# Kernel optimization log

Hardware: AMD Instinct MI355X
Metric: run time of the kernel (lower is better)

## Reference

```python
import jax, jax.numpy as jnp
import numpy as np

N_NODES = 50000
N_EDGES = 800000
FEAT_DIM = 64
NUM_RELS = 8


def setup_inputs() -> dict:
    key = jax.random.key(0)
    k1, k2, k3, k4, k5 = jax.random.split(key, 5)
    features = jax.random.normal(k1, (N_NODES, FEAT_DIM), dtype=jnp.float32)
    # xavier_uniform with relu gain ~= sqrt(2)*sqrt(6/(D+D))
    limit = np.sqrt(2.0) * np.sqrt(6.0 / (FEAT_DIM + FEAT_DIM))
    weight_r = jax.random.uniform(k2, (NUM_RELS, FEAT_DIM, FEAT_DIM), dtype=jnp.float32,
                                  minval=-limit, maxval=limit)
    src = jax.random.randint(k3, (N_EDGES,), 0, N_NODES, dtype=jnp.int64 if jax.config.jax_enable_x64 else jnp.int32)
    dst = jax.random.randint(k4, (N_EDGES,), 0, N_NODES, dtype=src.dtype)
    etype = jax.random.randint(k5, (N_EDGES,), 0, NUM_RELS, dtype=src.dtype)
    return {"features": features, "weight_r": weight_r, "src": src, "dst": dst, "etype": etype}


def reference(features, weight_r, src, dst, etype):
    N, D = features.shape
    c = 0.2
    # in-degree of each destination node (DGL 'deg' node data)
    deg = jax.ops.segment_sum(jnp.ones(dst.shape, dtype=features.dtype), dst, num_segments=N)
    # relation-batched matmul: h @ W_r for every relation, then gather per edge.
    # [R, N, D] = 8*50000*64 floats -- cheap vs. materializing [E, D, D] weights.
    hw = jnp.einsum('nd,rdf->rnf', features, weight_r)
    msg = hw[etype, src] / deg[dst][:, None]          # [E, D]
    M = jax.ops.segment_sum(msg, dst, num_segments=N)  # scatter-sum mailbox reduce
    updated = jax.nn.relu(c * features + (1.0 - c) * M)
    # DGL only applies reduce to nodes that received messages; others keep h.
    return jnp.where((deg > 0)[:, None], updated, features)
```

## Files before the change

### kernel.cpp

```cpp
#include <hip/hip_runtime.h>
#include <hip/hip_bf16.h>

#define N_NODES 50000
#define N_EDGES 800000
#define FEAT 64
#define NRELS 8
#define NBUCK 391
#define NBP 196
#define BCAP 2816
#define FB_BLOCKS 782
#define NPB 32
#define FUSE_BLOCKS 1563

typedef __attribute__((ext_vector_type(8))) short bf16x8;
typedef __attribute__((ext_vector_type(4))) float f32x4;

static __host__ __device__ inline size_t align256(size_t x) { return (x + 255) & ~(size_t)255; }

__device__ inline unsigned short f2b(float f) {
    unsigned u = __builtin_bit_cast(unsigned, f);
    unsigned r = (u + 0x7fffu + ((u >> 16) & 1u)) >> 16;
    return (unsigned short)r;
}
__device__ inline float b2f(unsigned short u) {
    unsigned v = ((unsigned)u) << 16;
    return __builtin_bit_cast(float, v);
}

__global__ void bfill_kernel(const int* __restrict__ dst, const int* __restrict__ srcv,
                             const int* __restrict__ et, const float* __restrict__ W,
                             const float* __restrict__ feat,
                             int* __restrict__ bcnt, int* __restrict__ tmp,
                             unsigned short* __restrict__ WtT,
                             unsigned short* __restrict__ Fb, int E, int N) {
    const int t = threadIdx.x;

    if (blockIdx.x >= NBP) {
        const int fbb = blockIdx.x - NBP;
        if (fbb < 32) {
            int i4 = fbb * 256 + t;
            float4 v = ((const float4*)W)[i4];
            int bse = i4 * 4;
            int f0 = bse & 63;
            int rd = bse >> 6;
            int d  = rd & 63;
            int r  = rd >> 6;
            unsigned short* w0 = WtT + ((size_t)(r * 64 + f0) * 64 + d);
            w0[0 * 64] = f2b(v.x);
            w0[1 * 64] = f2b(v.y);
            w0[2 * 64] = f2b(v.z);
            w0[3 * 64] = f2b(v.w);
        }
        const int node = fbb * 64 + (t >> 2);
        if (node >= N) return;
        const int seg = t & 3;
        const float4* F4 = (const float4*)feat + (size_t)node * 16 + seg * 4;
        float4 v0 = F4[0], v1 = F4[1], v2 = F4[2], v3 = F4[3];
        bf16x8 b0, b1;
        b0[0] = (short)f2b(v0.x); b0[1] = (short)f2b(v0.y);
        b0[2] = (short)f2b(v0.z); b0[3] = (short)f2b(v0.w);
        b0[4] = (short)f2b(v1.x); b0[5] = (short)f2b(v1.y);
        b0[6] = (short)f2b(v1.z); b0[7] = (short)f2b(v1.w);
        b1[0] = (short)f2b(v2.x); b1[1] = (short)f2b(v2.y);
        b1[2] = (short)f2b(v2.z); b1[3] = (short)f2b(v2.w);
        b1[4] = (short)f2b(v3.x); b1[5] = (short)f2b(v3.y);
        b1[6] = (short)f2b(v3.z); b1[7] = (short)f2b(v3.w);
        *(bf16x8*)(Fb + (size_t)node * 64 + seg * 16)     = b0;
        *(bf16x8*)(Fb + (size_t)node * 64 + seg * 16 + 8) = b1;
        return;
    }

    __shared__ int hist[392];
    __shared__ int base[392];
    __shared__ int lcur[392];
    for (int j = t; j < 392; j += 256) { hist[j] = 0; lcur[j] = 0; }
    __syncthreads();

    const int4* dst4 = (const int4*)dst;
    const int4* src4 = (const int4*)srcv;
    const int4* et4  = (const int4*)et;
    const int n4 = E >> 2;
    int bk[16], pk[16];
#pragma unroll
    for (int k = 0; k < 4; k++) {
        int i4 = blockIdx.x * 1024 + t + k * 256;
        if (i4 < n4) {
            int4 d = dst4[i4];
            int4 s = src4[i4];
            int4 r = et4[i4];
            const int dd[4] = {d.x, d.y, d.z, d.w};
            const int ss[4] = {s.x, s.y, s.z, s.w};
            const int rr[4] = {r.x, r.y, r.z, r.w};
#pragma unroll
            for (int j = 0; j < 4; j++) {
                int idx = k * 4 + j;
                bk[idx] = dd[j] >> 7;
                pk[idx] = (ss[j] & 0xFFFF) | (rr[j] << 16) | ((dd[j] & 127) << 19);
                atomicAdd(&hist[bk[idx]], 1);
            }
        } else {
#pragma unroll
            for (int j = 0; j < 4; j++) bk[k * 4 + j] = -1;
        }
    }
    __syncthreads();
    for (int j = t; j < NBUCK; j += 256)
        if (hist[j] > 0)
            base[j] = j * BCAP + atomicAdd(&bcnt[j], hist[j]);
    __syncthreads();
#pragma unroll
    for (int k = 0; k < 16; k++) {
        if (bk[k] >= 0) {
            int r = atomicAdd(&lcur[bk[k]], 1);
            int pos = base[bk[k]] + r;
            if (pos < (bk[k] + 1) * BCAP)
                tmp[pos] = pk[k];
        }
    }
}

__global__ void mid_kernel(const int* __restrict__ bcnt, const int* __restrict__ tmp,
                           int* __restrict__ spk, int* __restrict__ off_s,
                           int* __restrict__ off_e, int N) {
    __shared__ int hist[1024];
    __shared__ int s[256];
    const int t = threadIdx.x;

    const int b = blockIdx.x;
    const int n0 = b * 128;
    const int nn = min(128, N - n0);
    const int s0 = b * BCAP;
    const int s1 = s0 + min(bcnt[b], BCAP);

    *(int4*)&hist[t * 4] = make_int4(0, 0, 0, 0);
    __syncthreads();
    for (int i = s0 + t; i < s1; i += 1024) {
        int v0 = tmp[i];
        int v1 = (i + 256 < s1) ? tmp[i + 256] : -1;
        int v2 = (i + 512 < s1) ? tmp[i + 512] : -1;
        int v3 = (i + 768 < s1) ? tmp[i + 768] : -1;
        atomicAdd(&hist[(v0 >> 16) & 1023], 1);
        if (v1 >= 0) atomicAdd(&hist[(v1 >> 16) & 1023], 1);
        if (v2 >= 0) atomicAdd(&hist[(v2 >> 16) & 1023], 1);
        if (v3 >= 0) atomicAdd(&hist[(v3 >> 16) & 1023], 1);
    }
    __syncthreads();
    int loc[4], st4[4], T = 0;
#pragma unroll
    for (int j = 0; j < 4; j++) loc[j] = hist[t * 4 + j];
#pragma unroll
    for (int j = 0; j < 4; j++) { st4[j] = T; T += loc[j]; }
    s[t] = T;
    __syncthreads();
    for (int o = 1; o < 256; o <<= 1) {
        int u = (t >= o) ? s[t - o] : 0;
        __syncthreads();
        s[t] += u;
        __syncthreads();
    }
    const int ex = s[t] - T;
    {
        const int n = t >> 1;
        if (n < nn) {
            if ((t & 1) == 0) off_s[n0 + n] = s0 + ex;
            else              off_e[n0 + n] = s0 + ex + T;
        }
    }
#pragma unroll
    for (int j = 0; j < 4; j++) hist[t * 4 + j] = s0 + ex + st4[j];
    __syncthreads();
    for (int i = s0 + t; i < s1; i += 1024) {
        int v0 = tmp[i];
        int v1 = (i + 256 < s1) ? tmp[i + 256] : -1;
        int v2 = (i + 512 < s1) ? tmp[i + 512] : -1;
        int v3 = (i + 768 < s1) ? tmp[i + 768] : -1;
        int p0 = atomicAdd(&hist[(v0 >> 16) & 1023], 1);
        spk[p0] = v0;
        if (v1 >= 0) { int p1 = atomicAdd(&hist[(v1 >> 16) & 1023], 1); spk[p1] = v1; }
        if (v2 >= 0) { int p2 = atomicAdd(&hist[(v2 >> 16) & 1023], 1); spk[p2] = v2; }
        if (v3 >= 0) { int p3 = atomicAdd(&hist[(v3 >> 16) & 1023], 1); spk[p3] = v3; }
    }
}

__global__ __launch_bounds__(256, 4) void fuse_kernel(
    const int* __restrict__ off_s, const int* __restrict__ off_e,
    const int* __restrict__ spk, const unsigned short* __restrict__ Fb,
    const unsigned short* __restrict__ WtT, const float* __restrict__ feat,
    float* __restrict__ out, int N) {
    __shared__ unsigned short Sb[NRELS][NPB][64];
    const int t = threadIdx.x;
    const int n0 = blockIdx.x * NPB;
    const int nn = min(NPB, N - n0);
    const int gid = t >> 3, q = t & 7;
    const int lanebase = (t & 63) & ~7;

    int b = 0, e = 0;
    if (gid < nn) {
        const int gn = n0 + gid;
        b = off_s[gn];
        e = off_e[gn];
    }

    float4 h0e = make_float4(0.f, 0.f, 0.f, 0.f), h1e = h0e;
    const int ef0 = q * 8;
    if (gid < nn) {
        const float4* fp = (const float4*)feat + (size_t)(n0 + gid) * 16 + (ef0 >> 2);
        h0e = fp[0];
        h1e = fp[1];
    }

    {
        f32x4 z = {0.f, 0.f, 0.f, 0.f};
        f32x4* zp = (f32x4*)&Sb[0][0][0];
#pragma unroll
        for (int i = 0; i < 8; i++) zp[t + 256 * i] = z;
    }
    __syncthreads();

    if (gid < nn && b < e) {
        const int swz = (q ^ (gid & 7)) * 8;
        unsigned short* srow = &Sb[0][0][0] + (size_t)gid * 64 + swz;
        float a[8] = {0.f, 0.f, 0.f, 0.f, 0.f, 0.f, 0.f, 0.f};
        int curR = -1;

        auto flushS = [&](int rel) {
            bf16x8 v;
#pragma unroll
            for (int k = 0; k < 8; k++) v[k] = (short)f2b(a[k]);
            *(bf16x8*)(srow + (size_t)rel * (NPB * 64)) = v;
        };

        int pks[4];
#pragma unroll
        for (int k = 0; k < 4; k++)
            pks[k] = (b + q + 8 * k < e) ? spk[b + q + 8 * k] : -1;

        bf16x8 u[8];
        int pkv[8];
#pragma unroll
        for (int j = 0; j < 8; j++) {
            int pk = __shfl(pks[0], lanebase | j);
            pkv[j] = pk;
            u[j] = (bf16x8){0, 0, 0, 0, 0, 0, 0, 0};
            if (pk >= 0)
                u[j] = *(const bf16x8*)(Fb + (size_t)(pk & 0xFFFF) * 64 + q * 8);
        }
#pragma unroll
        for (int tier = 0; tier < 4; tier++) {
            if (b + tier * 8 >= e) break;
#pragma unroll
            for (int jj = 0; jj < 8; jj++) {
                const int j = tier * 8 + jj;
                bf16x8 uu = u[jj];
                int pk = pkv[jj];
                if (tier < 3) {
                    int pkn = __shfl(pks[(j + 8) >> 3], lanebase | jj);
                    pkv[jj] = pkn;
                    if (pkn >= 0)
                        u[jj] = *(const bf16x8*)(Fb + (size_t)(pkn & 0xFFFF) * 64 + q * 8);
                }
                if (pk >= 0) {
                    int rel = (pk >> 16) & 7;
                    if (rel != curR) {
                        if (curR >= 0) flushS(curR);
                        curR = rel;
#pragma unroll
                        for (int k = 0; k < 8; k++) a[k] = b2f((unsigned short)uu[k]);
                    } else {
#pragma unroll
                        for (int k = 0; k < 8; k++) a[k] += b2f((unsigned short)uu[k]);
                    }
                }
            }
        }
        for (int i = b + 32; i < e; i++) {
            int pk = spk[i];
            bf16x8 uu = *(const bf16x8*)(Fb + (size_t)(pk & 0xFFFF) * 64 + q * 8);
            int rel = (pk >> 16) & 7;
            if (rel != curR) {
                if (curR >= 0) flushS(curR);
                curR = rel;
#pragma unroll
                for (int k = 0; k < 8; k++) a[k] = b2f((unsigned short)uu[k]);
            } else {
#pragma unroll
                for (int k = 0; k < 8; k++) a[k] += b2f((unsigned short)uu[k]);
            }
        }
        if (curR >= 0) flushS(curR);
    }
    __syncthreads();

    const int w = t >> 6, l = t & 63, col = l & 15, quad = l >> 4;
    f32x4 acc0 = {0.f, 0.f, 0.f, 0.f}, acc1 = {0.f, 0.f, 0.f, 0.f};
    const int sw0 = (quad ^ (col & 7)) * 8;
    const int sw1 = ((quad + 4) ^ (col & 7)) * 8;
#pragma unroll
    for (int r = 0; r < NRELS; r++) {
        const unsigned short* wp = WtT + (size_t)r * 4096 + ((w * 16 + col) * 64 + quad * 8);
        bf16x8 b0 = *(const bf16x8*)wp;
        bf16x8 b1 = *(const bf16x8*)(wp + 32);
        const unsigned short* Sr = &Sb[0][0][0] + (size_t)r * (NPB * 64);
        bf16x8 a0 = *(const bf16x8*)&Sr[col * 64 + sw0];
        bf16x8 a1 = *(const bf16x8*)&Sr[col * 64 + sw1];
        bf16x8 c0 = *(const bf16x8*)&Sr[(16 + col) * 64 + sw0];
        bf16x8 c1 = *(const bf16x8*)&Sr[(16 + col) * 64 + sw1];
        acc0 = __builtin_amdgcn_mfma_f32_16x16x32_bf16(a0, b0, acc0, 0, 0, 0);
        acc0 = __builtin_amdgcn_mfma_f32_16x16x32_bf16(a1, b1, acc0, 0, 0, 0);
        acc1 = __builtin_amdgcn_mfma_f32_16x16x32_bf16(c0, b0, acc1, 0, 0, 0);
        acc1 = __builtin_amdgcn_mfma_f32_16x16x32_bf16(c1, b1, acc1, 0, 0, 0);
    }
    __syncthreads();

    float* C = (float*)&Sb[0][0][0];
#pragma unroll
    for (int i = 0; i < 4; i++) {
        C[(quad * 4 + i) * 72 + w * 16 + col]        = acc0[i];
        C[(16 + quad * 4 + i) * 72 + w * 16 + col]   = acc1[i];
    }
    __syncthreads();

    if (gid < nn) {
        const int gn = n0 + gid;
        const int deg = e - b;
        float4 m0 = *(const float4*)&C[gid * 72 + ef0];
        float4 m1 = *(const float4*)&C[gid * 72 + ef0 + 4];
        float4 r0, r1;
        if (deg > 0) {
            float inv = 0.8f / (float)deg;
            r0.x = fmaxf(0.2f * h0e.x + m0.x * inv, 0.f);
            r0.y = fmaxf(0.2f * h0e.y + m0.y * inv, 0.f);
            r0.z = fmaxf(0.2f * h0e.z + m0.z * inv, 0.f);
            r0.w = fmaxf(0.2f * h0e.w + m0.w * inv, 0.f);
            r1.x = fmaxf(0.2f * h1e.x + m1.x * inv, 0.f);
            r1.y = fmaxf(0.2f * h1e.y + m1.y * inv, 0.f);
            r1.z = fmaxf(0.2f * h1e.z + m1.z * inv, 0.f);
            r1.w = fmaxf(0.2f * h1e.w + m1.w * inv, 0.f);
        } else {
            r0 = h0e; r1 = h1e;
        }
        float4* op = (float4*)out + (size_t)gn * 16 + (ef0 >> 2);
        op[0] = r0;
        op[1] = r1;
    }
}

__global__ void degf_kernel(const int* __restrict__ dst, float* __restrict__ deg, int E) {
    int e = blockIdx.x * blockDim.x + threadIdx.x;
    if (e < E) atomicAdd(deg + dst[e], 1.0f);
}

__global__ void otf_kernel(const int* __restrict__ src, const int* __restrict__ dst,
                           const int* __restrict__ et, const float* __restrict__ feat,
                           const float* __restrict__ W, float* __restrict__ out, int E) {
    int wid = (blockIdx.x * blockDim.x + threadIdx.x) >> 6;
    int l = threadIdx.x & 63;
    if (wid >= E) return;
    int s = src[wid], dd = dst[wid], r = et[wid];
    float fv = feat[(size_t)s * 64 + l];
    const float* Wr = W + (size_t)r * 4096;
    float acc = 0.f;
#pragma unroll
    for (int d = 0; d < 64; d++) {
        float a = __shfl(fv, d);
        acc += a * Wr[d * 64 + l];
    }
    atomicAdd(out + (size_t)dd * 64 + l, acc);
}

__global__ void final_kernel(const float* __restrict__ feat, const float* __restrict__ deg,
                             float* __restrict__ out, int N) {
    int i = blockIdx.x * blockDim.x + threadIdx.x;
    if (i >= N * 16) return;
    int n = i >> 4;
    float d = deg[n];
    float4 f = ((const float4*)feat)[i];
    float4 m = ((float4*)out)[i];
    float4 res;
    if (d > 0.f) {
        float inv = 0.8f / d;
        res.x = fmaxf(0.2f * f.x + m.x * inv, 0.f);
        res.y = fmaxf(0.2f * f.y + m.y * inv, 0.f);
        res.z = fmaxf(0.2f * f.z + m.z * inv, 0.f);
        res.w = fmaxf(0.2f * f.w + m.w * inv, 0.f);
    } else {
        res = f;
    }
    ((float4*)out)[i] = res;
}

extern "C" void kernel_launch(void* const* d_in, const int* in_sizes, int n_in,
                              void* d_out, int out_size, void* d_ws, size_t ws_size,
                              hipStream_t stream) {
    const float* feat = (const float*)d_in[0];
    const float* W    = (const float*)d_in[1];
    const int*   src  = (const int*)d_in[2];
    const int*   dst  = (const int*)d_in[3];
    const int*   et   = (const int*)d_in[4];
    float* out = (float*)d_out;

    const int N = N_NODES, E = N_EDGES;

    char* p = (char*)d_ws;
    int* bcnt  = (int*)p;  p += align256((size_t)NBUCK * 4);
    int* off_s = (int*)p;  p += align256((size_t)N * 4);
    int* off_e = (int*)p;  p += align256((size_t)N * 4);
    int* tmp   = (int*)p;  p += align256((size_t)NBUCK * BCAP * 4);
    int* spk   = (int*)p;  p += align256((size_t)NBUCK * BCAP * 4);
    unsigned short* WtT = (unsigned short*)p;
    p += align256((size_t)NRELS * FEAT * FEAT * 2);
    unsigned short* Fb = (unsigned short*)p;
    p += align256((size_t)N * FEAT * 2);
    size_t need_full = (size_t)(p - (char*)d_ws);

    if (ws_size >= need_full) {
        hipMemsetAsync(bcnt, 0, (size_t)NBUCK * 4, stream);
        bfill_kernel<<<NBP + FB_BLOCKS, 256, 0, stream>>>(dst, src, et, W, feat,
                                                          bcnt, tmp, WtT, Fb, E, N);
        mid_kernel<<<NBUCK, 256, 0, stream>>>(bcnt, tmp, spk, off_s, off_e, N);
        fuse_kernel<<<FUSE_BLOCKS, 256, 0, stream>>>(off_s, off_e, spk, Fb, WtT,
                                                     feat, out, N);
    } else {
        float* deg = (float*)d_ws;
        hipMemsetAsync(out, 0, (size_t)N * FEAT * 4, stream);
        hipMemsetAsync(deg, 0, (size_t)N * 4, stream);
        degf_kernel<<<(E + 255) / 256, 256, 0, stream>>>(dst, deg, E);
        otf_kernel<<<(E + 3) / 4, 256, 0, stream>>>(src, dst, et, feat, W, out, E);
        final_kernel<<<(N * 16 + 255) / 256, 256, 0, stream>>>(feat, deg, out, N);
    }
}
```

Before: 129.9 us.

## Fuse per-bucket counting sort into aggregation kernel with 32-node buckets

Buckets shrink to 32 destination nodes each, which matches the fused block size. The separate mid_kernel counting sort is removed: each fuse block now reads its bucket from tmp, histograms by (node, relation) in shared memory, scatters the edges into an LDS edge list, and aggregates directly. This drops one kernel launch and the global round trip through spk/off arrays. The cost is a larger per-block LDS footprint and more shared-memory atomics on 1563 buckets in bfill. BCAP=768 per bucket could overflow for a skewed dst distribution, and edges past the cap would be silently dropped.

```diff
diff --git a/kernel.cpp b/kernel.cpp
--- a/kernel.cpp
+++ b/kernel.cpp
@@ -5,12 +5,11 @@
 #define N_EDGES 800000
 #define FEAT 64
 #define NRELS 8
-#define NBUCK 391
+#define NPB 32
+#define NBUCK 1563
 #define NBP 196
-#define BCAP 2816
+#define BCAP 768
 #define FB_BLOCKS 782
-#define NPB 32
-#define FUSE_BLOCKS 1563
 
 typedef __attribute__((ext_vector_type(8))) short bf16x8;
 typedef __attribute__((ext_vector_type(4))) float f32x4;
@@ -70,10 +69,10 @@
         return;
     }
 
-    __shared__ int hist[392];
-    __shared__ int base[392];
-    __shared__ int lcur[392];
-    for (int j = t; j < 392; j += 256) { hist[j] = 0; lcur[j] = 0; }
+    __shared__ int hist[NBUCK];
+    __shared__ int base[NBUCK];
+    __shared__ int lcur[NBUCK];
+    for (int j = t; j < NBUCK; j += 256) { hist[j] = 0; lcur[j] = 0; }
     __syncthreads();
 
     const int4* dst4 = (const int4*)dst;
@@ -94,8 +93,8 @@
 #pragma unroll
             for (int j = 0; j < 4; j++) {
                 int idx = k * 4 + j;
-                bk[idx] = dd[j] >> 7;
-                pk[idx] = (ss[j] & 0xFFFF) | (rr[j] << 16) | ((dd[j] & 127) << 19);
+                bk[idx] = dd[j] >> 5;
+                pk[idx] = (ss[j] & 0xFFFF) | (rr[j] << 16) | ((dd[j] & 31) << 19);
                 atomicAdd(&hist[bk[idx]], 1);
             }
         } else {
@@ -119,86 +118,117 @@
     }
 }
 
-__global__ void mid_kernel(const int* __restrict__ bcnt, const int* __restrict__ tmp,
-                           int* __restrict__ spk, int* __restrict__ off_s,
-                           int* __restrict__ off_e, int N) {
-    __shared__ int hist[1024];
-    __shared__ int s[256];
-    const int t = threadIdx.x;
-
-    const int b = blockIdx.x;
-    const int n0 = b * 128;
-    const int nn = min(128, N - n0);
-    const int s0 = b * BCAP;
-    const int s1 = s0 + min(bcnt[b], BCAP);
-
-    *(int4*)&hist[t * 4] = make_int4(0, 0, 0, 0);
-    __syncthreads();
-    for (int i = s0 + t; i < s1; i += 1024) {
-        int v0 = tmp[i];
-        int v1 = (i + 256 < s1) ? tmp[i + 256] : -1;
-        int v2 = (i + 512 < s1) ? tmp[i + 512] : -1;
-        int v3 = (i + 768 < s1) ? tmp[i + 768] : -1;
-        atomicAdd(&hist[(v0 >> 16) & 1023], 1);
-        if (v1 >= 0) atomicAdd(&hist[(v1 >> 16) & 1023], 1);
-        if (v2 >= 0) atomicAdd(&hist[(v2 >> 16) & 1023], 1);
-        if (v3 >= 0) atomicAdd(&hist[(v3 >> 16) & 1023], 1);
-    }
-    __syncthreads();
-    int loc[4], st4[4], T = 0;
-#pragma unroll
-    for (int j = 0; j < 4; j++) loc[j] = hist[t * 4 + j];
-#pragma unroll
-    for (int j = 0; j < 4; j++) { st4[j] = T; T += loc[j]; }
-    s[t] = T;
-    __syncthreads();
-    for (int o = 1; o < 256; o <<= 1) {
-        int u = (t >= o) ? s[t - o] : 0;
-        __syncthreads();
-        s[t] += u;
-        __syncthreads();
-    }
-    const int ex = s[t] - T;
-    {
-        const int n = t >> 1;
-        if (n < nn) {
-            if ((t & 1) == 0) off_s[n0 + n] = s0 + ex;
-            else              off_e[n0 + n] = s0 + ex + T;
-        }
-    }
-#pragma unroll
-    for (int j = 0; j < 4; j++) hist[t * 4 + j] = s0 + ex + st4[j];
-    __syncthreads();
-    for (int i = s0 + t; i < s1; i += 1024) {
-        int v0 = tmp[i];
-        int v1 = (i + 256 < s1) ? tmp[i + 256] : -1;
-        int v2 = (i + 512 < s1) ? tmp[i + 512] : -1;
-        int v3 = (i + 768 < s1) ? tmp[i + 768] : -1;
-        int p0 = atomicAdd(&hist[(v0 >> 16) & 1023], 1);
-        spk[p0] = v0;
-        if (v1 >= 0) { int p1 = atomicAdd(&hist[(v1 >> 16) & 1023], 1); spk[p1] = v1; }
-        if (v2 >= 0) { int p2 = atomicAdd(&hist[(v2 >> 16) & 1023], 1); spk[p2] = v2; }
-        if (v3 >= 0) { int p3 = atomicAdd(&hist[(v3 >> 16) & 1023], 1); spk[p3] = v3; }
-    }
-}
-
 __global__ __launch_bounds__(256, 4) void fuse_kernel(
-    const int* __restrict__ off_s, const int* __restrict__ off_e,
-    const int* __restrict__ spk, const unsigned short* __restrict__ Fb,
+    const int* __restrict__ bcnt, const int* __restrict__ tmp,
+    const unsigned short* __restrict__ Fb,
     const unsigned short* __restrict__ WtT, const float* __restrict__ feat,
     float* __restrict__ out, int N) {
     __shared__ unsigned short Sb[NRELS][NPB][64];
+    __shared__ int sedge[BCAP];
+    __shared__ int hist[256];
+    __shared__ int noff[NPB + 1];
     const int t = threadIdx.x;
-    const int n0 = blockIdx.x * NPB;
+    const int bkt = blockIdx.x;
+    const int n0 = bkt * NPB;
     const int nn = min(NPB, N - n0);
     const int gid = t >> 3, q = t & 7;
-    const int lanebase = (t & 63) & ~7;
+
+    {
+        f32x4 z = {0.f, 0.f, 0.f, 0.f};
+        f32x4* zp = (f32x4*)&Sb[0][0][0];
+#pragma unroll
+        for (int i = 0; i < 8; i++) zp[t + 256 * i] = z;
+    }
+
+    const int cnt = min(bcnt[bkt], BCAP);
+    const int* tb = tmp + (size_t)bkt * BCAP;
+    hist[t] = 0;
+    __syncthreads();
+    int v0 = (t < cnt) ? tb[t] : -1;
+    int v1 = (t + 256 < cnt) ? tb[t + 256] : -1;
+    int v2 = (t + 512 < cnt) ? tb[t + 512] : -1;
+    if (v0 >= 0) atomicAdd(&hist[(v0 >> 16) & 255], 1);
+    if (v1 >= 0) atomicAdd(&hist[(v1 >> 16) & 255], 1);
+    if (v2 >= 0) atomicAdd(&hist[(v2 >> 16) & 255], 1);
+    __syncthreads();
+    const int myc = hist[t];
+    for (int o = 1; o < 256; o <<= 1) {
+        int u_ = (t >= o) ? hist[t - o] : 0;
+        __syncthreads();
+        hist[t] += u_;
+        __syncthreads();
+    }
+    const int ex = hist[t] - myc;
+    if ((t & 7) == 0) noff[t >> 3] = ex;
+    if (t == 255) noff[NPB] = ex + myc;
+    __syncthreads();
+    hist[t] = ex;
+    __syncthreads();
+    if (v0 >= 0) { int p = atomicAdd(&hist[(v0 >> 16) & 255], 1); sedge[p] = v0; }
+    if (v1 >= 0) { int p = atomicAdd(&hist[(v1 >> 16) & 255], 1); sedge[p] = v1; }
+    if (v2 >= 0) { int p = atomicAdd(&hist[(v2 >> 16) & 255], 1); sedge[p] = v2; }
+    __syncthreads();
 
     int b = 0, e = 0;
-    if (gid < nn) {
-        const int gn = n0 + gid;
-        b = off_s[gn];
-        e = off_e[gn];
+    if (gid < nn) { b = noff[gid]; e = noff[gid + 1]; }
+    if (gid < nn && b < e) {
+        const int swz = (q ^ (gid & 7)) * 8;
+        unsigned short* srow = &Sb[0][0][0] + (size_t)gid * 64 + swz;
+        float a[8] = {0.f, 0.f, 0.f, 0.f, 0.f, 0.f, 0.f, 0.f};
+        int curR = -1;
+
+        auto flushS = [&](int rel) {
+            bf16x8 v;
+#pragma unroll
+            for (int k = 0; k < 8; k++) v[k] = (short)f2b(a[k]);
+            *(bf16x8*)(srow + (size_t)rel * (NPB * 64)) = v;
+        };
+
+        int pkj[32];
+#pragma unroll
+        for (int j = 0; j < 32; j++) pkj[j] = (b + j < e) ? sedge[b + j] : -1;
+
+        bf16x8 u[8];
+#pragma unroll
+        for (int j = 0; j < 8; j++) {
+            u[j] = (bf16x8){0, 0, 0, 0, 0, 0, 0, 0};
+            if (pkj[j] >= 0)
+                u[j] = *(const bf16x8*)(Fb + (size_t)(pkj[j] & 0xFFFF) * 64 + q * 8);
+        }
+#pragma unroll
+        for (int j = 0; j < 32; j++) {
+            bf16x8 uu = u[j & 7];
+            if (j + 8 < 32 && pkj[j + 8] >= 0)
+                u[j & 7] = *(const bf16x8*)(Fb + (size_t)(pkj[j + 8] & 0xFFFF) * 64 + q * 8);
+            int pk = pkj[j];
+            if (pk >= 0) {
+                int rel = (pk >> 16) & 7;
+                if (rel != curR) {
+                    if (curR >= 0) flushS(curR);
+                    curR = rel;
+#pragma unroll
+                    for (int k = 0; k < 8; k++) a[k] = b2f((unsigned short)uu[k]);
+                } else {
+#pragma unroll
+                    for (int k = 0; k < 8; k++) a[k] += b2f((unsigned short)uu[k]);
+                }
+            }
+        }
+        for (int i = b + 32; i < e; i++) {
+            int pk = sedge[i];
+            bf16x8 uu = *(const bf16x8*)(Fb + (size_t)(pk & 0xFFFF) * 64 + q * 8);
+            int rel = (pk >> 16) & 7;
+            if (rel != curR) {
+                if (curR >= 0) flushS(curR);
+                curR = rel;
+#pragma unroll
+                for (int k = 0; k < 8; k++) a[k] = b2f((unsigned short)uu[k]);
+            } else {
+#pragma unroll
+                for (int k = 0; k < 8; k++) a[k] += b2f((unsigned short)uu[k]);
+            }
+        }
+        if (curR >= 0) flushS(curR);
     }
 
     float4 h0e = make_float4(0.f, 0.f, 0.f, 0.f), h1e = h0e;
@@ -207,87 +237,6 @@
         const float4* fp = (const float4*)feat + (size_t)(n0 + gid) * 16 + (ef0 >> 2);
         h0e = fp[0];
         h1e = fp[1];
-    }
-
-    {
-        f32x4 z = {0.f, 0.f, 0.f, 0.f};
-        f32x4* zp = (f32x4*)&Sb[0][0][0];
-#pragma unroll
-        for (int i = 0; i < 8; i++) zp[t + 256 * i] = z;
-    }
-    __syncthreads();
-
-    if (gid < nn && b < e) {
-        const int swz = (q ^ (gid & 7)) * 8;
-        unsigned short* srow = &Sb[0][0][0] + (size_t)gid * 64 + swz;
-        float a[8] = {0.f, 0.f, 0.f, 0.f, 0.f, 0.f, 0.f, 0.f};
-        int curR = -1;
-
-        auto flushS = [&](int rel) {
-            bf16x8 v;
-#pragma unroll
-            for (int k = 0; k < 8; k++) v[k] = (short)f2b(a[k]);
-            *(bf16x8*)(srow + (size_t)rel * (NPB * 64)) = v;
-        };
-
-        int pks[4];
-#pragma unroll
-        for (int k = 0; k < 4; k++)
-            pks[k] = (b + q + 8 * k < e) ? spk[b + q + 8 * k] : -1;
-
-        bf16x8 u[8];
-        int pkv[8];
-#pragma unroll
-        for (int j = 0; j < 8; j++) {
-            int pk = __shfl(pks[0], lanebase | j);
-            pkv[j] = pk;
-            u[j] = (bf16x8){0, 0, 0, 0, 0, 0, 0, 0};
-            if (pk >= 0)
-                u[j] = *(const bf16x8*)(Fb + (size_t)(pk & 0xFFFF) * 64 + q * 8);
-        }
-#pragma unroll
-        for (int tier = 0; tier < 4; tier++) {
-            if (b + tier * 8 >= e) break;
-#pragma unroll
-            for (int jj = 0; jj < 8; jj++) {
-                const int j = tier * 8 + jj;
-                bf16x8 uu = u[jj];
-                int pk = pkv[jj];
-                if (tier < 3) {
-                    int pkn = __shfl(pks[(j + 8) >> 3], lanebase | jj);
-                    pkv[jj] = pkn;
-                    if (pkn >= 0)
-                        u[jj] = *(const bf16x8*)(Fb + (size_t)(pkn & 0xFFFF) * 64 + q * 8);
-                }
-                if (pk >= 0) {
-                    int rel = (pk >> 16) & 7;
-                    if (rel != curR) {
-                        if (curR >= 0) flushS(curR);
-                        curR = rel;
-#pragma unroll
-                        for (int k = 0; k < 8; k++) a[k] = b2f((unsigned short)uu[k]);
-                    } else {
-#pragma unroll
-                        for (int k = 0; k < 8; k++) a[k] += b2f((unsigned short)uu[k]);
-                    }
-                }
-            }
-        }
-        for (int i = b + 32; i < e; i++) {
-            int pk = spk[i];
-            bf16x8 uu = *(const bf16x8*)(Fb + (size_t)(pk & 0xFFFF) * 64 + q * 8);
-            int rel = (pk >> 16) & 7;
-            if (rel != curR) {
-                if (curR >= 0) flushS(curR);
-                curR = rel;
-#pragma unroll
-                for (int k = 0; k < 8; k++) a[k] = b2f((unsigned short)uu[k]);
-            } else {
-#pragma unroll
-                for (int k = 0; k < 8; k++) a[k] += b2f((unsigned short)uu[k]);
-            }
-        }
-        if (curR >= 0) flushS(curR);
     }
     __syncthreads();
 
@@ -403,10 +352,7 @@
 
     char* p = (char*)d_ws;
     int* bcnt  = (int*)p;  p += align256((size_t)NBUCK * 4);
-    int* off_s = (int*)p;  p += align256((size_t)N * 4);
-    int* off_e = (int*)p;  p += align256((size_t)N * 4);
     int* tmp   = (int*)p;  p += align256((size_t)NBUCK * BCAP * 4);
-    int* spk   = (int*)p;  p += align256((size_t)NBUCK * BCAP * 4);
     unsigned short* WtT = (unsigned short*)p;
     p += align256((size_t)NRELS * FEAT * FEAT * 2);
     unsigned short* Fb = (unsigned short*)p;
@@ -417,9 +363,7 @@
         hipMemsetAsync(bcnt, 0, (size_t)NBUCK * 4, stream);
         bfill_kernel<<<NBP + FB_BLOCKS, 256, 0, stream>>>(dst, src, et, W, feat,
                                                           bcnt, tmp, WtT, Fb, E, N);
-        mid_kernel<<<NBUCK, 256, 0, stream>>>(bcnt, tmp, spk, off_s, off_e, N);
-        fuse_kernel<<<FUSE_BLOCKS, 256, 0, stream>>>(off_s, off_e, spk, Fb, WtT,
-                                                     feat, out, N);
+        fuse_kernel<<<NBUCK, 256, 0, stream>>>(bcnt, tmp, Fb, WtT, feat, out, N);
     } else {
         float* deg = (float*)d_ws;
         hipMemsetAsync(out, 0, (size_t)N * FEAT * 4, stream);
```

After: 125.0 us. -3.8%, faster.
